# Kernel optimization log

Hardware: AMD Instinct MI355X
Metric: run time of the kernel (lower is better)

## Reference

```python
import jax, jax.numpy as jnp
import numpy as np

EPS = 1e-5

def _ln(x, g, b):
    mu = jnp.mean(x, axis=-1, keepdims=True)
    var = jnp.mean((x - mu) ** 2, axis=-1, keepdims=True)
    return (x - mu) / jnp.sqrt(var + EPS) * g + b

def _silu(x):
    return x * jax.nn.sigmoid(x)

def setup_inputs() -> dict:
    key = jax.random.key(0)
    ks = jax.random.split(key, 32)
    B = 131072
    def rn(k, shape, scale=0.05):
        return jax.random.normal(k, shape, dtype=jnp.float32) * scale
    inp = {
        'x': jax.random.normal(ks[0], (B, 90), dtype=jnp.float32),
        'w_emb': rn(ks[1], (24, 10)),
        'pos_d': rn(ks[2], (9, 24), 0.02),
        'pos_c': rn(ks[3], (3, 64), 0.02),
        'tw1': rn(ks[4], (256, 72)), 'tb1': rn(ks[5], (256,)),
        'tw2': rn(ks[6], (256, 256)), 'tb2': rn(ks[7], (256,)),
        'tw3': rn(ks[8], (64, 256)), 'tb3': jnp.zeros((64,), jnp.float32),
        'ln1g': jnp.ones((64,), jnp.float32), 'ln1b': jnp.zeros((64,), jnp.float32),
        'inpw': rn(ks[9], (192, 64)), 'inpb': rn(ks[10], (192,)),
        'outw': rn(ks[11], (64, 64)), 'outb': rn(ks[12], (64,)),
        'ln2g': jnp.ones((64,), jnp.float32), 'ln2b': jnp.zeros((64,), jnp.float32),
        'ffw1': rn(ks[13], (128, 64)), 'ffb1': rn(ks[14], (128,)),
        'ffw2': rn(ks[15], (64, 128)), 'ffb2': rn(ks[16], (64,)),
        'hw1': rn(ks[17], (160, 192)), 'hb1': rn(ks[18], (160,)),
        'hw2': rn(ks[19], (64, 160)), 'hb2': rn(ks[20], (64,)),
        'hw3': rn(ks[21], (1, 64)), 'hb3': jnp.zeros((1,), jnp.float32),
    }
    return inp

def reference(x, w_emb, pos_d, pos_c, tw1, tb1, tw2, tb2, tw3, tb3,
              ln1g, ln1b, inpw, inpb, outw, outb, ln2g, ln2b,
              ffw1, ffb1, ffw2, ffb2, hw1, hb1, hw2, hb2, hw3, hb3):
    B = x.shape[0]
    H, D = 4, 16  # heads, head_dim (embed 64)
    digits = x.reshape(B, 9, 10) @ w_emb.T + pos_d          # [B,9,24]
    chunks = digits.reshape(B, 3, 72)                        # [B,3,72]
    h = _silu(chunks @ tw1.T + tb1)                          # [B,3,256]
    h = _silu(h @ tw2.T + tb2)                               # [B,3,256]
    chunks = h @ tw3.T + tb3                                 # [B,3,64]
    chunks = chunks + pos_c
    a = _ln(chunks, ln1g, ln1b)
    qkv = a @ inpw.T + inpb                                  # [B,3,192]
    q, k, v = jnp.split(qkv, 3, axis=-1)
    q = q.reshape(B, 3, H, D).transpose(0, 2, 1, 3)
    k = k.reshape(B, 3, H, D).transpose(0, 2, 1, 3)
    v = v.reshape(B, 3, H, D).transpose(0, 2, 1, 3)
    scores = jnp.einsum('bhsd,bhtd->bhst', q, k) / jnp.sqrt(jnp.float32(D))
    attn = jax.nn.softmax(scores, axis=-1)
    o = jnp.einsum('bhst,bhtd->bhsd', attn, v)
    o = o.transpose(0, 2, 1, 3).reshape(B, 3, 64)
    attn_out = o @ outw.T + outb
    chunks = chunks + attn_out
    f = _ln(chunks, ln2g, ln2b)
    chunks = chunks + (_silu(f @ ffw1.T + ffb1) @ ffw2.T + ffb2)
    flat = chunks.reshape(B, 192)
    hh = _silu(flat @ hw1.T + hb1)
    hh = _silu(hh @ hw2.T + hb2)
    return hh @ hw3.T + hb3                                  # [B,1]
```

## Files before the change

### kernel.cpp

```cpp
#include <hip/hip_runtime.h>
#include <math.h>


typedef short s8v __attribute__((ext_vector_type(8)));
typedef float f4v __attribute__((ext_vector_type(4)));
typedef int   i2v __attribute__((ext_vector_type(2)));
typedef int   i4v __attribute__((ext_vector_type(4)));

__device__ __forceinline__ short f2bf(float f) {
    unsigned u = __float_as_uint(f);
    unsigned r = (u + 0x7fffu + ((u >> 16) & 1u)) >> 16;
    return (short)r;
}
__device__ __forceinline__ int cvt_pk_bf16(float a, float b) {
    int r;
    asm("v_cvt_pk_bf16_f32 %0, %1, %2" : "=v"(r) : "v"(a), "v"(b));
    return r;
}
__device__ __forceinline__ float silu_f(float v) {
    return v * __builtin_amdgcn_rcpf(1.0f + __expf(-v));
}

#define BARRIER() do {                                        \
    asm volatile("s_waitcnt lgkmcnt(0)" ::: "memory");        \
    __builtin_amdgcn_s_barrier();                             \
    __builtin_amdgcn_sched_barrier(0);                        \
} while (0)

#define OFF_BD   0
#define OFF_TW1  3072
#define OFF_TW2  27648
#define OFF_TW3  93184
#define OFF_INP  109568
#define OFF_OUT  121856
#define OFF_FF1  125952
#define OFF_FF2  134144
#define OFF_HW1  142336
#define OFF_HW2  173056

__global__ void pack_weights(const float* __restrict__ w_emb,
                             const float* __restrict__ tw1, const float* __restrict__ tw2,
                             const float* __restrict__ tw3, const float* __restrict__ inpw,
                             const float* __restrict__ outw, const float* __restrict__ ffw1,
                             const float* __restrict__ ffw2, const float* __restrict__ hw1,
                             const float* __restrict__ hw2, short* __restrict__ dst)
{
    int L = blockIdx.y;
    const float* W; int K, KS, N, off;
    switch (L) {
      case 0: W = w_emb; K = 32;  KS = 1; N = 96;  off = OFF_BD;  break;
      case 1: W = tw1;   K = 72;  KS = 3; N = 256; off = OFF_TW1; break;
      case 2: W = tw2;   K = 256; KS = 8; N = 256; off = OFF_TW2; break;
      case 3: W = tw3;   K = 256; KS = 8; N = 64;  off = OFF_TW3; break;
      case 4: W = inpw;  K = 64;  KS = 2; N = 192; off = OFF_INP; break;
      case 5: W = outw;  K = 64;  KS = 2; N = 64;  off = OFF_OUT; break;
      case 6: W = ffw1;  K = 64;  KS = 2; N = 128; off = OFF_FF1; break;
      case 7: W = ffw2;  K = 128; KS = 4; N = 64;  off = OFF_FF2; break;
      case 8: W = hw1;   K = 192; KS = 6; N = 160; off = OFF_HW1; break;
      default:W = hw2;   K = 160; KS = 5; N = 64;  off = OFF_HW2; break;
    }
    int total = (N >> 4) * KS * 512;
    for (int e = blockIdx.x * blockDim.x + threadIdx.x; e < total; e += gridDim.x * blockDim.x) {
        int nt = e / (KS * 512);
        int r  = e - nt * (KS * 512);
        int ks = r >> 9;
        int q  = r & 511;
        int l  = q >> 3, j = q & 7;
        int n  = nt * 16 + (l & 15);
        int k  = ks * 32 + (l >> 4) * 8 + j;
        float v;
        if (L == 0) {
            int gl = n / 24, jj = n - gl * 24, kk = k - gl * 10;
            v = (n < 72 && kk >= 0 && kk < 10) ? w_emb[jj * 10 + kk] : 0.0f;
        } else {
            v = (k < K) ? W[n * K + k] : 0.0f;
        }
        dst[off + e] = f2bf(v);
    }
}

template<int KSH> struct PreW { s8v w[KSH]; };

template<int KSH>
__device__ __forceinline__ PreW<KSH> preloadW(const short* __restrict__ Wp,
                                              int lane, int nt, int ksTotal) {
    PreW<KSH> p;
    #pragma unroll
    for (int ks = 0; ks < KSH; ++ks)
        p.w[ks] = *(const s8v*)(Wp + nt * (ksTotal * 512) + ks * 512 + lane * 8);
    return p;
}

template<int EPI>
__device__ __forceinline__ void epi_store(f4v acc, f4v bv, int t, int n0, void* Out, int Op,
                                          const float* __restrict__ aux)
{
    if (EPI == 0 || EPI == 1) {
        float v0 = acc[0] + bv[0], v1 = acc[1] + bv[1];
        float v2 = acc[2] + bv[2], v3 = acc[3] + bv[3];
        if (EPI == 0) { v0 = silu_f(v0); v1 = silu_f(v1); v2 = silu_f(v2); v3 = silu_f(v3); }
        i2v pk; pk[0] = cvt_pk_bf16(v0, v1); pk[1] = cvt_pk_bf16(v2, v3);
        *(i2v*)((short*)Out + t * Op + n0) = pk;
    } else if (EPI == 2) {
        f4v* p = (f4v*)((float*)Out + t * Op + n0);
        f4v o = *p;
        #pragma unroll
        for (int i = 0; i < 4; ++i) o[i] += acc[i] + bv[i];
        *p = o;
    } else if (EPI == 3) {
        f4v pc = *(const f4v*)(aux + (t % 3) * 64 + n0);
        f4v o;
        #pragma unroll
        for (int i = 0; i < 4; ++i) o[i] = acc[i] + bv[i] + pc[i];
        *(f4v*)((float*)Out + t * Op + n0) = o;
    } else if (EPI == 4) {
        i2v pk;
        if (n0 < 72) {
            f4v pd = *(const f4v*)(aux + (t % 3) * 72 + n0);
            pk[0] = cvt_pk_bf16(acc[0] + pd[0], acc[1] + pd[1]);
            pk[1] = cvt_pk_bf16(acc[2] + pd[2], acc[3] + pd[3]);
        } else { pk[0] = 0; pk[1] = 0; }
        *(i2v*)((short*)Out + t * Op + n0) = pk;
    } else if (EPI == 5) {
        f4v ch = *(const f4v*)(aux + t * 68 + n0);
        int rr = t / 3, cc = t - rr * 3;
        i2v pk;
        pk[0] = cvt_pk_bf16(ch[0] + acc[0] + bv[0], ch[1] + acc[1] + bv[1]);
        pk[1] = cvt_pk_bf16(ch[2] + acc[2] + bv[2], ch[3] + acc[3] + bv[3]);
        *(i2v*)((short*)Out + rr * Op + cc * 64 + n0) = pk;
    } else {
        f4v w = *(const f4v*)(aux + n0);
        float p = silu_f(acc[0] + bv[0]) * w[0] + silu_f(acc[1] + bv[1]) * w[1]
                + silu_f(acc[2] + bv[2]) * w[2] + silu_f(acc[3] + bv[3]) * w[3];
        ((float*)Out)[t * Op + (n0 >> 2)] = p;
    }
}

template<int MT, int KS, int EPI>
__device__ __forceinline__ void mfma_T(
    const short* __restrict__ Wp,
    const float* __restrict__ bias,
    const short* A, int Ap, void* Out, int Op, int N,
    const float* __restrict__ aux, int lane, int wid, PreW<KS> pre)
{
    const int l15 = lane & 15, l4 = lane >> 4;
    s8v xf[MT][KS];
    #pragma unroll
    for (int m = 0; m < MT; ++m)
        #pragma unroll
        for (int ks = 0; ks < KS; ++ks)
            xf[m][ks] = *(const s8v*)(A + (m * 16 + l15) * Ap + ks * 32 + l4 * 8);

    s8v wf[KS];
    #pragma unroll
    for (int ks = 0; ks < KS; ++ks) wf[ks] = pre.w[ks];

    const int NT = N >> 4;
    for (int nt = wid; nt < NT; nt += 4) {
        s8v wfn[KS];
        const bool more = (nt + 4) < NT;
        if (more) {
            #pragma unroll
            for (int ks = 0; ks < KS; ++ks)
                wfn[ks] = *(const s8v*)(Wp + (nt + 4) * (KS * 512) + ks * 512 + lane * 8);
        }
        const int n0 = nt * 16 + l4 * 4;
        f4v bv = {0.f, 0.f, 0.f, 0.f};
        if (EPI != 4) bv = *(const f4v*)(bias + n0);
        #pragma unroll
        for (int m = 0; m < MT; ++m) {
            f4v acc = {0.f, 0.f, 0.f, 0.f};
            #pragma unroll
            for (int ks = 0; ks < KS; ++ks)
                acc = __builtin_amdgcn_mfma_f32_16x16x32_bf16(wf[ks], xf[m][ks], acc, 0, 0, 0);
            epi_store<EPI>(acc, bv, m * 16 + l15, n0, Out, Op, aux);
        }
        if (more) {
            #pragma unroll
            for (int ks = 0; ks < KS; ++ks) wf[ks] = wfn[ks];
        }
    }
}

template<int MT, int KSH, int KH, int NTW, int EPI>
__device__ __forceinline__ void mfma_acc(
    const short* __restrict__ Wp, const float* __restrict__ bias,
    const short* A, int Ap, void* Out, int Op,
    const float* __restrict__ aux, int lane, int wid, int ntBase, PreW<KSH> pre)
{
    const int l15 = lane & 15, l4 = lane >> 4;
    const int KS = KSH * KH;
    f4v acc[NTW][MT];
    #pragma unroll
    for (int i = 0; i < NTW; ++i)
        #pragma unroll
        for (int m = 0; m < MT; ++m) acc[i][m] = (f4v){0.f, 0.f, 0.f, 0.f};

    #pragma unroll
    for (int kh = 0; kh < KH; ++kh) {
        s8v xf[MT][KSH];
        #pragma unroll
        for (int m = 0; m < MT; ++m)
            #pragma unroll
            for (int ks = 0; ks < KSH; ++ks)
                xf[m][ks] = *(const s8v*)(A + (m * 16 + l15) * Ap + (kh * KSH + ks) * 32 + l4 * 8);
        #pragma unroll
        for (int i = 0; i < NTW; ++i) {
            const int nt = wid + (ntBase + i) * 4;
            s8v wf[KSH];
            if (kh == 0 && i == 0) {
                #pragma unroll
                for (int ks = 0; ks < KSH; ++ks) wf[ks] = pre.w[ks];
            } else {
                #pragma unroll
                for (int ks = 0; ks < KSH; ++ks)
                    wf[ks] = *(const s8v*)(Wp + nt * (KS * 512) + (kh * KSH + ks) * 512 + lane * 8);
            }
            #pragma unroll
            for (int m = 0; m < MT; ++m)
                #pragma unroll
                for (int ks = 0; ks < KSH; ++ks)
                    acc[i][m] = __builtin_amdgcn_mfma_f32_16x16x32_bf16(wf[ks], xf[m][ks], acc[i][m], 0, 0, 0);
        }
    }
    #pragma unroll
    for (int i = 0; i < NTW; ++i) {
        const int nt = wid + (ntBase + i) * 4;
        const int n0 = nt * 16 + l4 * 4;
        f4v bv = *(const f4v*)(bias + n0);
        #pragma unroll
        for (int m = 0; m < MT; ++m)
            epi_store<EPI>(acc[i][m], bv, m * 16 + l15, n0, Out, Op, aux);
    }
}

__device__ __forceinline__ void ln_phase(const float* CH, short* dst, int dp,
                                         const float* __restrict__ g,
                                         const float* __restrict__ b, int tid)
{
    if (tid < 192) {
        int t = tid >> 2, p = tid & 3;
        const float* cp = CH + t * 68 + p * 16;
        f4v c[4];
        #pragma unroll
        for (int i = 0; i < 4; ++i) c[i] = *(const f4v*)(cp + i * 4);
        float s = 0.f, ss = 0.f;
        #pragma unroll
        for (int i = 0; i < 4; ++i)
            #pragma unroll
            for (int j = 0; j < 4; ++j) { float v = c[i][j]; s += v; ss += v * v; }
        s += __shfl_xor(s, 1); ss += __shfl_xor(ss, 1);
        s += __shfl_xor(s, 2); ss += __shfl_xor(ss, 2);
        float mu = s * (1.0f / 64.0f);
        float var = ss * (1.0f / 64.0f) - mu * mu;
        float rstd = rsqrtf(var + 1e-5f);
        int pk[8];
        #pragma unroll
        for (int i = 0; i < 4; ++i) {
            f4v gv = *(const f4v*)(g + p * 16 + i * 4);
            f4v bvv = *(const f4v*)(b + p * 16 + i * 4);
            float o0 = (c[i][0] - mu) * rstd * gv[0] + bvv[0];
            float o1 = (c[i][1] - mu) * rstd * gv[1] + bvv[1];
            float o2 = (c[i][2] - mu) * rstd * gv[2] + bvv[2];
            float o3 = (c[i][3] - mu) * rstd * gv[3] + bvv[3];
            pk[i * 2]     = cvt_pk_bf16(o0, o1);
            pk[i * 2 + 1] = cvt_pk_bf16(o2, o3);
        }
        i4v w0 = {pk[0], pk[1], pk[2], pk[3]};
        i4v w1 = {pk[4], pk[5], pk[6], pk[7]};
        *(i4v*)(dst + t * dp + p * 16) = w0;
        *(i4v*)(dst + t * dp + p * 16 + 8) = w1;
    }
}

#define ARENA 25344
#define LDS_BYTES (2 * ARENA)

__global__ __launch_bounds__(256, 3)
void towers_mfma(const float* __restrict__ x,
                 const float* __restrict__ pos_d, const float* __restrict__ pos_c,
                 const float* __restrict__ tb1, const float* __restrict__ tb2,
                 const float* __restrict__ tb3,
                 const float* __restrict__ ln1g, const float* __restrict__ ln1b,
                 const float* __restrict__ inpb, const float* __restrict__ outb,
                 const float* __restrict__ ln2g, const float* __restrict__ ln2b,
                 const float* __restrict__ ffb1, const float* __restrict__ ffb2,
                 const float* __restrict__ hb1, const float* __restrict__ hb2,
                 const float* __restrict__ hw3, const float* __restrict__ hb3,
                 const short* __restrict__ wsBp,
                 float* __restrict__ out)
{
    __shared__ __align__(16) char smem[LDS_BYTES];
    char* P = smem;
    char* Q = smem + ARENA;

    const int tid = threadIdx.x;
    const int lane = tid & 63, wid = tid >> 6;
    const long long row0 = (long long)blockIdx.x * 16;

    short* A0 = (short*)Q;
    PreW<1> preBD = preloadW<1>(wsBp + OFF_BD, lane, wid, 1);
    {
        const float* gx = x + row0 * 90;
        for (int i = tid; i < 720; i += 256) {
            int r = i / 45, p = i - r * 45;
            int c = p / 15, kk = (p - c * 15) * 2;
            float2 v = *(const float2*)(gx + r * 90 + p * 2);
            *(int*)(A0 + (r * 3 + c) * 40 + kk) = cvt_pk_bf16(v.x, v.y);
        }
        for (int i = tid; i < 48; i += 256)
            *(int*)(A0 + i * 40 + 30) = 0;
    }
    BARRIER();

    short* A1 = (short*)P;
    mfma_T<3, 1, 4>(wsBp + OFF_BD, nullptr, A0, 40, A1, 104, 96, pos_d, lane, wid, preBD);
    PreW<3> preT1 = preloadW<3>(wsBp + OFF_TW1, lane, wid, 3);
    BARRIER();

    short* H1 = (short*)Q;
    short* H2 = (short*)P;
    float* CH = (float*)Q;
    mfma_T<3, 3, 0>(wsBp + OFF_TW1, tb1, A1, 104, H1, 264, 256, nullptr, lane, wid, preT1);
    PreW<4> preT2 = preloadW<4>(wsBp + OFF_TW2, lane, wid, 8);
    BARRIER();
    mfma_acc<3, 4, 2, 2, 0>(wsBp + OFF_TW2, tb2, H1, 264, H2, 264, nullptr, lane, wid, 0, preT2);
    {
        PreW<4> preT2b = preloadW<4>(wsBp + OFF_TW2, lane, wid + 8, 8);
        mfma_acc<3, 4, 2, 2, 0>(wsBp + OFF_TW2, tb2, H1, 264, H2, 264, nullptr, lane, wid, 2, preT2b);
    }
    PreW<4> preT3 = preloadW<4>(wsBp + OFF_TW3, lane, wid, 8);
    BARRIER();
    mfma_acc<3, 4, 2, 1, 3>(wsBp + OFF_TW3, tb3, H2, 264, CH, 68, pos_c, lane, wid, 0, preT3);
    PreW<2> preINP = preloadW<2>(wsBp + OFF_INP, lane, wid, 2);
    BARRIER();

    short* aln = (short*)(Q + 13056);
    ln_phase(CH, aln, 72, ln1g, ln1b, tid);
    BARRIER();

    short* qkv = (short*)P;
    mfma_T<3, 2, 1>(wsBp + OFF_INP, inpb, aln, 72, qkv, 200, 192, nullptr, lane, wid, preINP);
    PreW<2> preOUT = preloadW<2>(wsBp + OFF_OUT, lane, wid, 2);
    BARRIER();

    short* ao = (short*)(Q + 13056);
    if (tid < 192) {
        int r = tid & 15, hc = tid >> 4;
        int h = hc & 3, cq = hc >> 2;
        const short* qp = qkv + (r * 3 + cq) * 200 + h * 16;
        float qv[16];
        { s8v q0 = *(const s8v*)qp, q1 = *(const s8v*)(qp + 8);
          #pragma unroll
          for (int j = 0; j < 8; ++j) {
              qv[j] = __uint_as_float(((unsigned)(unsigned short)q0[j]) << 16);
              qv[8 + j] = __uint_as_float(((unsigned)(unsigned short)q1[j]) << 16);
          } }
        float sc[3];
        #pragma unroll
        for (int c = 0; c < 3; ++c) {
            const short* kp = qkv + (r * 3 + c) * 200 + 64 + h * 16;
            s8v k0 = *(const s8v*)kp, k1 = *(const s8v*)(kp + 8);
            float acc = 0.f;
            #pragma unroll
            for (int j = 0; j < 8; ++j) {
                acc += qv[j] * __uint_as_float(((unsigned)(unsigned short)k0[j]) << 16)
                     + qv[8 + j] * __uint_as_float(((unsigned)(unsigned short)k1[j]) << 16);
            }
            sc[c] = acc * 0.25f;
        }
        float m = fmaxf(sc[0], fmaxf(sc[1], sc[2]));
        float e0 = __expf(sc[0] - m), e1 = __expf(sc[1] - m), e2 = __expf(sc[2] - m);
        float inv = 1.0f / (e0 + e1 + e2);
        e0 *= inv; e1 *= inv; e2 *= inv;
        float ov[16];
        #pragma unroll
        for (int j = 0; j < 16; ++j) ov[j] = 0.f;
        const float ee[3] = {e0, e1, e2};
        #pragma unroll
        for (int c = 0; c < 3; ++c) {
            const short* vp = qkv + (r * 3 + c) * 200 + 128 + h * 16;
            s8v v0 = *(const s8v*)vp, v1 = *(const s8v*)(vp + 8);
            #pragma unroll
            for (int j = 0; j < 8; ++j) {
                ov[j]     += ee[c] * __uint_as_float(((unsigned)(unsigned short)v0[j]) << 16);
                ov[8 + j] += ee[c] * __uint_as_float(((unsigned)(unsigned short)v1[j]) << 16);
            }
        }
        short* op = ao + (r * 3 + cq) * 72 + h * 16;
        i4v pk;
        pk[0] = cvt_pk_bf16(ov[0], ov[1]);   pk[1] = cvt_pk_bf16(ov[2], ov[3]);
        pk[2] = cvt_pk_bf16(ov[4], ov[5]);   pk[3] = cvt_pk_bf16(ov[6], ov[7]);
        *(i4v*)op = pk;
        pk[0] = cvt_pk_bf16(ov[8], ov[9]);   pk[1] = cvt_pk_bf16(ov[10], ov[11]);
        pk[2] = cvt_pk_bf16(ov[12], ov[13]); pk[3] = cvt_pk_bf16(ov[14], ov[15]);
        *(i4v*)(op + 8) = pk;
    }
    BARRIER();

    mfma_T<3, 2, 2>(wsBp + OFF_OUT, outb, ao, 72, CH, 68, 64, nullptr, lane, wid, preOUT);
    PreW<2> preFF1 = preloadW<2>(wsBp + OFF_FF1, lane, wid, 2);
    BARRIER();

    short* fb = (short*)(Q + 13056);
    ln_phase(CH, fb, 72, ln2g, ln2b, tid);
    BARRIER();

    short* g1 = (short*)P;
    mfma_T<3, 2, 0>(wsBp + OFF_FF1, ffb1, fb, 72, g1, 136, 128, nullptr, lane, wid, preFF1);
    PreW<4> preFF2 = preloadW<4>(wsBp + OFF_FF2, lane, wid, 4);
    BARRIER();
    short* flat = (short*)(P + 13312);
    mfma_T<3, 4, 5>(wsBp + OFF_FF2, ffb2, g1, 136, flat, 200, 64, CH, lane, wid, preFF2);
    PreW<6> preH1 = preloadW<6>(wsBp + OFF_HW1, lane, wid, 6);
    BARRIER();

    short* hh1 = (short*)(Q + 13056);
    mfma_T<1, 6, 0>(wsBp + OFF_HW1, hb1, flat, 200, hh1, 168, 160, nullptr, lane, wid, preH1);
    PreW<5> preH2 = preloadW<5>(wsBp + OFF_HW2, lane, wid, 5);
    BARRIER();
    float* part = (float*)P;
    mfma_T<1, 5, 6>(wsBp + OFF_HW2, hb2, hh1, 168, part, 16, 64, hw3, lane, wid, preH2);
    BARRIER();

    if (tid < 64) {
        int r = tid >> 2, p = tid & 3;
        const float* pp = part + r * 16 + p * 4;
        float acc = pp[0] + pp[1] + pp[2] + pp[3];
        acc += __shfl_xor(acc, 1);
        acc += __shfl_xor(acc, 2);
        if (p == 0) out[row0 + r] = acc + hb3[0];
    }
}

extern "C" void kernel_launch(void* const* d_in, const int* in_sizes, int n_in,
                              void* d_out, int out_size, void* d_ws, size_t ws_size,
                              hipStream_t stream) {
    const float* x     = (const float*)d_in[0];
    const float* w_emb = (const float*)d_in[1];
    const float* pos_d = (const float*)d_in[2];
    const float* pos_c = (const float*)d_in[3];
    const float* tw1   = (const float*)d_in[4];
    const float* tb1   = (const float*)d_in[5];
    const float* tw2   = (const float*)d_in[6];
    const float* tb2   = (const float*)d_in[7];
    const float* tw3   = (const float*)d_in[8];
    const float* tb3   = (const float*)d_in[9];
    const float* ln1g  = (const float*)d_in[10];
    const float* ln1b  = (const float*)d_in[11];
    const float* inpw  = (const float*)d_in[12];
    const float* inpb  = (const float*)d_in[13];
    const float* outw  = (const float*)d_in[14];
    const float* outb  = (const float*)d_in[15];
    const float* ln2g  = (const float*)d_in[16];
    const float* ln2b  = (const float*)d_in[17];
    const float* ffw1  = (const float*)d_in[18];
    const float* ffb1  = (const float*)d_in[19];
    const float* ffw2  = (const float*)d_in[20];
    const float* ffb2  = (const float*)d_in[21];
    const float* hw1   = (const float*)d_in[22];
    const float* hb1   = (const float*)d_in[23];
    const float* hw2   = (const float*)d_in[24];
    const float* hb2   = (const float*)d_in[25];
    const float* hw3   = (const float*)d_in[26];
    const float* hb3   = (const float*)d_in[27];
    float* out = (float*)d_out;
    short* wsBp = (short*)d_ws;

    pack_weights<<<dim3(16, 10), 256, 0, stream>>>(w_emb, tw1, tw2, tw3, inpw, outw,
                                                   ffw1, ffw2, hw1, hw2, wsBp);

    const int B = in_sizes[0] / 90;
    towers_mfma<<<B / 16, 256, 0, stream>>>(
        x, pos_d, pos_c, tb1, tb2, tb3,
        ln1g, ln1b, inpb, outb, ln2g, ln2b,
        ffb1, ffb2, hb1, hb2, hw3, hb3, wsBp, out);
}
```

Baseline: 247.0 us.

## Fold digit embedding into first tower layer weights and per-position bias

Precomputes the product of tw1 and the block-diagonal digit embedding into a single 256x30 weight, and folds pos_d and tb1 into a per-chunk-position bias. The main kernel then skips the separate embedding MFMA stage and its barrier, feeding the raw digits directly into a K=32 matmul with a new silu epilogue that reads the position-dependent bias. The LDS buffer roles are swapped to match the removed stage. Folding the weights before rounding to bf16 changes rounding slightly, and the pack kernel does more serial work per element.

```diff
diff --git a/kernel.cpp b/kernel.cpp
--- a/kernel.cpp
+++ b/kernel.cpp
@@ -27,37 +27,64 @@
     __builtin_amdgcn_sched_barrier(0);                        \
 } while (0)
 
-#define OFF_BD   0
-#define OFF_TW1  3072
-#define OFF_TW2  27648
-#define OFF_TW3  93184
-#define OFF_INP  109568
-#define OFF_OUT  121856
-#define OFF_FF1  125952
-#define OFF_FF2  134144
-#define OFF_HW1  142336
-#define OFF_HW2  173056
-
-__global__ void pack_weights(const float* __restrict__ w_emb,
-                             const float* __restrict__ tw1, const float* __restrict__ tw2,
-                             const float* __restrict__ tw3, const float* __restrict__ inpw,
-                             const float* __restrict__ outw, const float* __restrict__ ffw1,
-                             const float* __restrict__ ffw2, const float* __restrict__ hw1,
-                             const float* __restrict__ hw2, short* __restrict__ dst)
+#define OFF_T1F  0
+#define OFF_TW2  8192
+#define OFF_TW3  73728
+#define OFF_INP  90112
+#define OFF_OUT  102400
+#define OFF_FF1  106496
+#define OFF_FF2  114688
+#define OFF_HW1  122880
+#define OFF_HW2  153600
+#define BIAS1_ELEM 163840
+
+__global__ void pack_weights(const float* __restrict__ w_emb, const float* __restrict__ tw1,
+                             const float* __restrict__ pos_d, const float* __restrict__ tb1,
+                             const float* __restrict__ tw2, const float* __restrict__ tw3,
+                             const float* __restrict__ inpw, const float* __restrict__ outw,
+                             const float* __restrict__ ffw1, const float* __restrict__ ffw2,
+                             const float* __restrict__ hw1, const float* __restrict__ hw2,
+                             short* __restrict__ dst)
 {
     int L = blockIdx.y;
+    if (L == 0) {
+        int total = 16 * 512;
+        for (int e = blockIdx.x * blockDim.x + threadIdx.x; e < total; e += gridDim.x * blockDim.x) {
+            int nt = e >> 9, q = e & 511;
+            int l = q >> 3, j = q & 7;
+            int n = nt * 16 + (l & 15);
+            int k = (l >> 4) * 8 + j;
+            float v = 0.f;
+            if (k < 30) {
+                int gl = k / 10, kk = k - gl * 10;
+                const float* trow = tw1 + n * 72 + gl * 24;
+                for (int jj = 0; jj < 24; ++jj) v += trow[jj] * w_emb[jj * 10 + kk];
+            }
+            dst[OFF_T1F + e] = f2bf(v);
+        }
+        return;
+    }
+    if (L == 9) {
+        float* b1 = (float*)(dst + BIAS1_ELEM);
+        for (int e = blockIdx.x * blockDim.x + threadIdx.x; e < 768; e += gridDim.x * blockDim.x) {
+            int pos = e >> 8, n = e & 255;
+            float v = tb1[n];
+            for (int j = 0; j < 72; ++j)
+                v += tw1[n * 72 + j] * pos_d[(pos * 3 + j / 24) * 24 + (j % 24)];
+            b1[e] = v;
+        }
+        return;
+    }
     const float* W; int K, KS, N, off;
     switch (L) {
-      case 0: W = w_emb; K = 32;  KS = 1; N = 96;  off = OFF_BD;  break;
-      case 1: W = tw1;   K = 72;  KS = 3; N = 256; off = OFF_TW1; break;
-      case 2: W = tw2;   K = 256; KS = 8; N = 256; off = OFF_TW2; break;
-      case 3: W = tw3;   K = 256; KS = 8; N = 64;  off = OFF_TW3; break;
-      case 4: W = inpw;  K = 64;  KS = 2; N = 192; off = OFF_INP; break;
-      case 5: W = outw;  K = 64;  KS = 2; N = 64;  off = OFF_OUT; break;
-      case 6: W = ffw1;  K = 64;  KS = 2; N = 128; off = OFF_FF1; break;
-      case 7: W = ffw2;  K = 128; KS = 4; N = 64;  off = OFF_FF2; break;
-      case 8: W = hw1;   K = 192; KS = 6; N = 160; off = OFF_HW1; break;
-      default:W = hw2;   K = 160; KS = 5; N = 64;  off = OFF_HW2; break;
+      case 1: W = tw2;  K = 256; KS = 8; N = 256; off = OFF_TW2; break;
+      case 2: W = tw3;  K = 256; KS = 8; N = 64;  off = OFF_TW3; break;
+      case 3: W = inpw; K = 64;  KS = 2; N = 192; off = OFF_INP; break;
+      case 4: W = outw; K = 64;  KS = 2; N = 64;  off = OFF_OUT; break;
+      case 5: W = ffw1; K = 64;  KS = 2; N = 128; off = OFF_FF1; break;
+      case 6: W = ffw2; K = 128; KS = 4; N = 64;  off = OFF_FF2; break;
+      case 7: W = hw1;  K = 192; KS = 6; N = 160; off = OFF_HW1; break;
+      default:W = hw2;  K = 160; KS = 5; N = 64;  off = OFF_HW2; break;
     }
     int total = (N >> 4) * KS * 512;
     for (int e = blockIdx.x * blockDim.x + threadIdx.x; e < total; e += gridDim.x * blockDim.x) {
@@ -68,14 +95,7 @@
         int l  = q >> 3, j = q & 7;
         int n  = nt * 16 + (l & 15);
         int k  = ks * 32 + (l >> 4) * 8 + j;
-        float v;
-        if (L == 0) {
-            int gl = n / 24, jj = n - gl * 24, kk = k - gl * 10;
-            v = (n < 72 && kk >= 0 && kk < 10) ? w_emb[jj * 10 + kk] : 0.0f;
-        } else {
-            v = (k < K) ? W[n * K + k] : 0.0f;
-        }
-        dst[off + e] = f2bf(v);
+        dst[off + e] = f2bf((k < K) ? W[n * K + k] : 0.0f);
     }
 }
 
@@ -113,14 +133,6 @@
         #pragma unroll
         for (int i = 0; i < 4; ++i) o[i] = acc[i] + bv[i] + pc[i];
         *(f4v*)((float*)Out + t * Op + n0) = o;
-    } else if (EPI == 4) {
-        i2v pk;
-        if (n0 < 72) {
-            f4v pd = *(const f4v*)(aux + (t % 3) * 72 + n0);
-            pk[0] = cvt_pk_bf16(acc[0] + pd[0], acc[1] + pd[1]);
-            pk[1] = cvt_pk_bf16(acc[2] + pd[2], acc[3] + pd[3]);
-        } else { pk[0] = 0; pk[1] = 0; }
-        *(i2v*)((short*)Out + t * Op + n0) = pk;
     } else if (EPI == 5) {
         f4v ch = *(const f4v*)(aux + t * 68 + n0);
         int rr = t / 3, cc = t - rr * 3;
@@ -128,11 +140,17 @@
         pk[0] = cvt_pk_bf16(ch[0] + acc[0] + bv[0], ch[1] + acc[1] + bv[1]);
         pk[1] = cvt_pk_bf16(ch[2] + acc[2] + bv[2], ch[3] + acc[3] + bv[3]);
         *(i2v*)((short*)Out + rr * Op + cc * 64 + n0) = pk;
-    } else {
+    } else if (EPI == 6) {
         f4v w = *(const f4v*)(aux + n0);
         float p = silu_f(acc[0] + bv[0]) * w[0] + silu_f(acc[1] + bv[1]) * w[1]
                 + silu_f(acc[2] + bv[2]) * w[2] + silu_f(acc[3] + bv[3]) * w[3];
         ((float*)Out)[t * Op + (n0 >> 2)] = p;
+    } else {
+        f4v bp = *(const f4v*)(aux + (t % 3) * 256 + n0);
+        float v0 = silu_f(acc[0] + bp[0]), v1 = silu_f(acc[1] + bp[1]);
+        float v2 = silu_f(acc[2] + bp[2]), v3 = silu_f(acc[3] + bp[3]);
+        i2v pk; pk[0] = cvt_pk_bf16(v0, v1); pk[1] = cvt_pk_bf16(v2, v3);
+        *(i2v*)((short*)Out + t * Op + n0) = pk;
     }
 }
 
@@ -166,7 +184,7 @@
         }
         const int n0 = nt * 16 + l4 * 4;
         f4v bv = {0.f, 0.f, 0.f, 0.f};
-        if (EPI != 4) bv = *(const f4v*)(bias + n0);
+        if (EPI != 7) bv = *(const f4v*)(bias + n0);
         #pragma unroll
         for (int m = 0; m < MT; ++m) {
             f4v acc = {0.f, 0.f, 0.f, 0.f};
@@ -278,9 +296,8 @@
 
 __global__ __launch_bounds__(256, 3)
 void towers_mfma(const float* __restrict__ x,
-                 const float* __restrict__ pos_d, const float* __restrict__ pos_c,
-                 const float* __restrict__ tb1, const float* __restrict__ tb2,
-                 const float* __restrict__ tb3,
+                 const float* __restrict__ pos_c,
+                 const float* __restrict__ tb2, const float* __restrict__ tb3,
                  const float* __restrict__ ln1g, const float* __restrict__ ln1b,
                  const float* __restrict__ inpb, const float* __restrict__ outb,
                  const float* __restrict__ ln2g, const float* __restrict__ ln2b,
@@ -297,9 +314,10 @@
     const int tid = threadIdx.x;
     const int lane = tid & 63, wid = tid >> 6;
     const long long row0 = (long long)blockIdx.x * 16;
+    const float* bias1 = (const float*)(wsBp + BIAS1_ELEM);
 
     short* A0 = (short*)Q;
-    PreW<1> preBD = preloadW<1>(wsBp + OFF_BD, lane, wid, 1);
+    PreW<1> preT1f = preloadW<1>(wsBp + OFF_T1F, lane, wid, 1);
     {
         const float* gx = x + row0 * 90;
         for (int i = tid; i < 720; i += 256) {
@@ -313,17 +331,12 @@
     }
     BARRIER();
 
-    short* A1 = (short*)P;
-    mfma_T<3, 1, 4>(wsBp + OFF_BD, nullptr, A0, 40, A1, 104, 96, pos_d, lane, wid, preBD);
-    PreW<3> preT1 = preloadW<3>(wsBp + OFF_TW1, lane, wid, 3);
-    BARRIER();
-
-    short* H1 = (short*)Q;
-    short* H2 = (short*)P;
-    float* CH = (float*)Q;
-    mfma_T<3, 3, 0>(wsBp + OFF_TW1, tb1, A1, 104, H1, 264, 256, nullptr, lane, wid, preT1);
+    short* H1 = (short*)P;
+    mfma_T<3, 1, 7>(wsBp + OFF_T1F, nullptr, A0, 40, H1, 264, 256, bias1, lane, wid, preT1f);
     PreW<4> preT2 = preloadW<4>(wsBp + OFF_TW2, lane, wid, 8);
     BARRIER();
+
+    short* H2 = (short*)Q;
     mfma_acc<3, 4, 2, 2, 0>(wsBp + OFF_TW2, tb2, H1, 264, H2, 264, nullptr, lane, wid, 0, preT2);
     {
         PreW<4> preT2b = preloadW<4>(wsBp + OFF_TW2, lane, wid + 8, 8);
@@ -331,20 +344,22 @@
     }
     PreW<4> preT3 = preloadW<4>(wsBp + OFF_TW3, lane, wid, 8);
     BARRIER();
+
+    float* CH = (float*)P;
     mfma_acc<3, 4, 2, 1, 3>(wsBp + OFF_TW3, tb3, H2, 264, CH, 68, pos_c, lane, wid, 0, preT3);
     PreW<2> preINP = preloadW<2>(wsBp + OFF_INP, lane, wid, 2);
     BARRIER();
 
-    short* aln = (short*)(Q + 13056);
+    short* aln = (short*)(P + 13056);
     ln_phase(CH, aln, 72, ln1g, ln1b, tid);
     BARRIER();
 
-    short* qkv = (short*)P;
+    short* qkv = (short*)Q;
     mfma_T<3, 2, 1>(wsBp + OFF_INP, inpb, aln, 72, qkv, 200, 192, nullptr, lane, wid, preINP);
     PreW<2> preOUT = preloadW<2>(wsBp + OFF_OUT, lane, wid, 2);
     BARRIER();
 
-    short* ao = (short*)(Q + 13056);
+    short* ao = (short*)(P + 13056);
     if (tid < 192) {
         int r = tid & 15, hc = tid >> 4;
         int h = hc & 3, cq = hc >> 2;
@@ -402,24 +417,24 @@
     PreW<2> preFF1 = preloadW<2>(wsBp + OFF_FF1, lane, wid, 2);
     BARRIER();
 
-    short* fb = (short*)(Q + 13056);
+    short* fb = (short*)(P + 13056);
     ln_phase(CH, fb, 72, ln2g, ln2b, tid);
     BARRIER();
 
-    short* g1 = (short*)P;
+    short* g1 = (short*)Q;
     mfma_T<3, 2, 0>(wsBp + OFF_FF1, ffb1, fb, 72, g1, 136, 128, nullptr, lane, wid, preFF1);
     PreW<4> preFF2 = preloadW<4>(wsBp + OFF_FF2, lane, wid, 4);
     BARRIER();
-    short* flat = (short*)(P + 13312);
+    short* flat = (short*)(Q + 13312);
     mfma_T<3, 4, 5>(wsBp + OFF_FF2, ffb2, g1, 136, flat, 200, 64, CH, lane, wid, preFF2);
     PreW<6> preH1 = preloadW<6>(wsBp + OFF_HW1, lane, wid, 6);
     BARRIER();
 
-    short* hh1 = (short*)(Q + 13056);
+    short* hh1 = (short*)(P + 13056);
     mfma_T<1, 6, 0>(wsBp + OFF_HW1, hb1, flat, 200, hh1, 168, 160, nullptr, lane, wid, preH1);
     PreW<5> preH2 = preloadW<5>(wsBp + OFF_HW2, lane, wid, 5);
     BARRIER();
-    float* part = (float*)P;
+    float* part = (float*)Q;
     mfma_T<1, 5, 6>(wsBp + OFF_HW2, hb2, hh1, 168, part, 16, 64, hw3, lane, wid, preH2);
     BARRIER();
 
@@ -467,12 +482,13 @@
     float* out = (float*)d_out;
     short* wsBp = (short*)d_ws;
 
-    pack_weights<<<dim3(16, 10), 256, 0, stream>>>(w_emb, tw1, tw2, tw3, inpw, outw,
+    pack_weights<<<dim3(16, 10), 256, 0, stream>>>(w_emb, tw1, pos_d, tb1,
+                                                   tw2, tw3, inpw, outw,
                                                    ffw1, ffw2, hw1, hw2, wsBp);
 
     const int B = in_sizes[0] / 90;
     towers_mfma<<<B / 16, 256, 0, stream>>>(
-        x, pos_d, pos_c, tb1, tb2, tb3,
+        x, pos_c, tb2, tb3,
         ln1g, ln1b, inpb, outb, ln2g, ln2b,
         ffb1, ffb2, hb1, hb2, hw3, hb3, wsBp, out);
 }
```

Result: faster. 228.3 us (-7.6%).
